# Kernel tuning notes

Measured on AMD Instinct MI355X. Metric: run time of the kernel, lower is better.

## Reference

```python
import jax, jax.numpy as jnp
import numpy as np

BATCH = 16384
NUM_FEATURES = 1024  # sum(field_dims)
CROSS_DIMS = NUM_FEATURES * (NUM_FEATURES - 1) // 2  # 523776


def setup_inputs() -> dict:
    key = jax.random.key(0)
    kx, kw = jax.random.split(key)
    x = jax.random.uniform(kx, (BATCH, NUM_FEATURES), dtype=jnp.float32)
    # xavier-uniform init of a (cross_dims, 1) parameter: bound = sqrt(6/(fan_in+fan_out))
    bound = float(np.sqrt(6.0 / (CROSS_DIMS + 1)))
    w = jax.random.uniform(kw, (CROSS_DIMS,), dtype=jnp.float32, minval=-bound, maxval=bound)
    return {"x": x, "w": w}


def reference(x, w):
    # POLY2: out_b = sigmoid( sum_{i<j} w_{ij} * x_{b,i} * x_{b,j} )
    # sklearn PolynomialFeatures(interaction_only) emits pairs in combinations
    # (row-major i<j) order, identical to triu_indices(k=1) ordering.
    F = x.shape[1]
    iu, ju = jnp.triu_indices(F, k=1)
    W = jnp.zeros((F, F), dtype=x.dtype).at[iu, ju].set(w)  # [F,F] strictly upper-tri
    # quadratic form without materializing the [B, F*(F-1)/2] pairwise matrix
    out = jnp.einsum('bi,ij,bj->b', x, W, x)  # [B]
    return jax.nn.sigmoid(out.astype(jnp.float32))
```

## Files before the change

kernel.cpp:

```cpp
#include <hip/hip_runtime.h>
#include <hip/hip_bf16.h>

#define F 1024
#define B_ROWS 16384

typedef short v8s __attribute__((ext_vector_type(8)));
typedef float v4f __attribute__((ext_vector_type(4)));
typedef unsigned short v8u __attribute__((ext_vector_type(8)));
typedef unsigned short ushort_t;

__device__ __forceinline__ unsigned short f2bf(float f) {
    unsigned int u = __builtin_bit_cast(unsigned int, f);
    u = (u + 0x7FFFu + ((u >> 16) & 1u)) >> 16;
    return (unsigned short)u;
}

__device__ __forceinline__ void gload_lds16(const ushort_t* g, ushort_t* l) {
    __builtin_amdgcn_global_load_lds(
        (const __attribute__((address_space(1))) unsigned int*)g,
        (__attribute__((address_space(3))) unsigned int*)l,
        16, 0, 0);
}


__global__ __launch_bounds__(256) void prep_kernel(
        const float* __restrict__ w, const float* __restrict__ x,
        ushort_t* __restrict__ Bp, ushort_t* __restrict__ Xp,
        float* __restrict__ acc) {
    const int bid  = blockIdx.x;
    const int tid  = threadIdx.x;
    const int lane = tid & 63;
    const int wave = tid >> 6;
    const int l16  = lane & 15;
    const int quad = lane >> 4;

    if (bid < 64) {
        acc[bid * 256 + tid] = 0.0f;
    } else if (bid < 576) {
        const int c  = (bid - 64) * 4 + wave;
        const int n  = (c >> 5) * 16 + l16;
        const int k0 = (c & 31) * 32 + quad * 8;
        v8u o;
#pragma unroll
        for (int e = 0; e < 8; ++e) {
            const int k = k0 + e;
            float v = 0.0f;
            if (k < n) {
                const int idx = k * (F - 1) - (k * (k - 1)) / 2 + (n - k - 1);
                v = w[idx];
            }
            o[e] = f2bf(v);
        }
        *(v8u*)(Bp + (size_t)c * 512 + lane * 8) = o;
    } else {
        const int c  = (bid - 576) * 4 + wave;
        const int r  = (c >> 5) * 16 + l16;
        const int k0 = (c & 31) * 32 + quad * 8;
        const float* src = x + (size_t)r * F + k0;
        float4 v0 = *(const float4*)(src);
        float4 v1 = *(const float4*)(src + 4);
        v8u o;
        o[0] = f2bf(v0.x); o[1] = f2bf(v0.y); o[2] = f2bf(v0.z); o[3] = f2bf(v0.w);
        o[4] = f2bf(v1.x); o[5] = f2bf(v1.y); o[6] = f2bf(v1.z); o[7] = f2bf(v1.w);
        *(v8u*)(Xp + (size_t)c * 512 + lane * 8) = o;
    }
}

__global__ __launch_bounds__(256, 3) void gemm_kernel(
        const ushort_t* __restrict__ Xp,
        const ushort_t* __restrict__ Bp,
        const float*   __restrict__ Xf,
        float*         __restrict__ rowacc) {
    __shared__ ushort_t Bs[2 * 16 * 512];

    const int f   = blockIdx.x;
    const int xcd = f & 7;
    const int g   = f >> 3;
    const int y   = g & 15;
    const int nt  = 7 - (g >> 4);
    const int blockM = (xcd * 16 + y) * 128;
    const int blockN = nt * 128;
    const int nch    = 2 * (nt + 1);

    const int tid   = threadIdx.x;
    const int lane  = tid & 63;
    const int wave  = tid >> 6;
    const int waveM = wave >> 1;
    const int waveN = wave & 1;
    const int quad  = lane >> 4;
    const int l16   = lane & 15;

    const int mg = (blockM >> 4) + waveM * 4;
    const v8s* A8 = (const v8s*)Xp + (size_t)mg * 32 * 64 + lane;

    const int q0   = wave * 4;
    const int ngB  = nt * 8;

#define STAGE_B(c, buf)                                                        \
    {                                                                          \
        _Pragma("unroll")                                                      \
        for (int q = 0; q < 4; ++q) {                                          \
            const int qq  = q0 + q;                                            \
            const int kgl = qq >> 3, ngl = qq & 7;                             \
            gload_lds16(Bp + (size_t)((ngB + ngl) * 32 + (c) * 2 + kgl) * 512 + lane * 8, \
                        Bs + (buf) * 8192 + (kgl * 8 + ngl) * 512);            \
        }                                                                      \
    }

    v4f acc[4][4];
#pragma unroll
    for (int i = 0; i < 4; i++)
#pragma unroll
        for (int j = 0; j < 4; j++) acc[i][j] = (v4f)(0.0f);

    v8s a0[4], a1[4], bfr[4];

    STAGE_B(0, 0)
#pragma unroll
    for (int mi = 0; mi < 4; ++mi) a0[mi] = A8[(mi * 32 + 0) * 64];
    __syncthreads();

    for (int c = 0; c < nch; ++c) {
        const int  buf  = c & 1;
        const bool more = (c + 1 < nch);
        if (more) STAGE_B(c + 1, buf ^ 1)

#pragma unroll
        for (int ni = 0; ni < 4; ++ni)
            bfr[ni] = *(const v8s*)(Bs + buf * 8192 + (0 * 8 + waveN * 4 + ni) * 512 + lane * 8);
#pragma unroll
        for (int mi = 0; mi < 4; ++mi) a1[mi] = A8[(mi * 32 + 2 * c + 1) * 64];
#pragma unroll
        for (int mi = 0; mi < 4; ++mi)
#pragma unroll
            for (int ni = 0; ni < 4; ++ni)
                acc[mi][ni] = __builtin_amdgcn_mfma_f32_16x16x32_bf16(
                    a0[mi], bfr[ni], acc[mi][ni], 0, 0, 0);

#pragma unroll
        for (int ni = 0; ni < 4; ++ni)
            bfr[ni] = *(const v8s*)(Bs + buf * 8192 + (1 * 8 + waveN * 4 + ni) * 512 + lane * 8);
        if (more) {
#pragma unroll
            for (int mi = 0; mi < 4; ++mi) a0[mi] = A8[(mi * 32 + 2 * c + 2) * 64];
        }
#pragma unroll
        for (int mi = 0; mi < 4; ++mi)
#pragma unroll
            for (int ni = 0; ni < 4; ++ni)
                acc[mi][ni] = __builtin_amdgcn_mfma_f32_16x16x32_bf16(
                    a1[mi], bfr[ni], acc[mi][ni], 0, 0, 0);

        if (more) __syncthreads();
    }
#undef STAGE_B

#pragma unroll
    for (int mi = 0; mi < 4; mi++) {
#pragma unroll
        for (int r = 0; r < 4; r++) {
            const int b = blockM + waveM * 64 + mi * 16 + quad * 4 + r;
            const float* xr = Xf + (size_t)b * F + blockN + waveN * 64 + l16;
            float pv = acc[mi][0][r] * xr[0]
                     + acc[mi][1][r] * xr[16]
                     + acc[mi][2][r] * xr[32]
                     + acc[mi][3][r] * xr[48];
            pv += __shfl_xor(pv, 1);
            pv += __shfl_xor(pv, 2);
            pv += __shfl_xor(pv, 4);
            pv += __shfl_xor(pv, 8);
            if (l16 == 0) atomicAdd(&rowacc[b], pv);
        }
    }
}

__global__ void sigmoid_kernel(const float* __restrict__ acc, float* __restrict__ out) {
    int b = blockIdx.x * blockDim.x + threadIdx.x;
    out[b] = 1.0f / (1.0f + __expf(-acc[b]));
}

__global__ void fallback_kernel(const float* __restrict__ x, const float* __restrict__ w,
                                float* __restrict__ out) {
    __shared__ float xs[F];
    __shared__ float partial[4];
    const int b = blockIdx.x;
    for (int i = threadIdx.x; i < F; i += 256) xs[i] = x[(size_t)b * F + i];
    __syncthreads();
    float s = 0.0f;
    for (int i = threadIdx.x; i < F - 1; i += 256) {
        const float xi = xs[i];
        const int kbase = i * (F - 1) - (i * (i - 1)) / 2 - i - 1;
        for (int j = i + 1; j < F; j++) s += w[kbase + j] * xi * xs[j];
    }
    for (int off = 32; off; off >>= 1) s += __shfl_down(s, off);
    if ((threadIdx.x & 63) == 0) partial[threadIdx.x >> 6] = s;
    __syncthreads();
    if (threadIdx.x == 0) {
        float t = partial[0] + partial[1] + partial[2] + partial[3];
        out[b] = 1.0f / (1.0f + __expf(-t));
    }
}

extern "C" void kernel_launch(void* const* d_in, const int* in_sizes, int n_in,
                              void* d_out, int out_size, void* d_ws, size_t ws_size,
                              hipStream_t stream) {
    const float* x = (const float*)d_in[0];
    const float* w = (const float*)d_in[1];
    float* out = (float*)d_out;

    const size_t acc_bytes = 65536;
    const size_t B_bytes   = (size_t)F * F * 2;
    const size_t Xp_bytes  = (size_t)B_ROWS * F * 2;
    const size_t needed = acc_bytes + B_bytes + Xp_bytes;

    if (ws_size < needed) {
        fallback_kernel<<<B_ROWS, 256, 0, stream>>>(x, w, out);
        return;
    }

    float*    acc = (float*)d_ws;
    ushort_t* Bp  = (ushort_t*)((char*)d_ws + acc_bytes);
    ushort_t* Xp  = (ushort_t*)((char*)d_ws + acc_bytes + B_bytes);

    prep_kernel<<<64 + 512 + 8192, 256, 0, stream>>>(w, x, Bp, Xp, acc);
    gemm_kernel<<<1024, 256, 0, stream>>>(Xp, Bp, x, acc);
    sigmoid_kernel<<<B_ROWS / 256, 256, 0, stream>>>(acc, out);
}
```

Before: 133.2 us.

## Fuse sigmoid into GEMM via last-block counter, relax barrier waits, raise occupancy

Removes the separate sigmoid kernel launch: each M row-block keeps a counter, and the last of its 8 N-tile blocks applies the sigmoid and writes the output. In the main loop, the full __syncthreads is replaced by a partial vmcnt wait plus s_barrier, with sched_barriers added to pin the instruction order. Launch bounds rise from 3 to 4 blocks per CU. The changes aim to save a launch and overlap more memory traffic, but they add atomics and fences and risk register spills under the tighter bound.

```diff
diff --git a/kernel.cpp b/kernel.cpp
--- a/kernel.cpp
+++ b/kernel.cpp
@@ -26,7 +26,7 @@
 __global__ __launch_bounds__(256) void prep_kernel(
         const float* __restrict__ w, const float* __restrict__ x,
         ushort_t* __restrict__ Bp, ushort_t* __restrict__ Xp,
-        float* __restrict__ acc) {
+        float* __restrict__ acc, int* __restrict__ cnt) {
     const int bid  = blockIdx.x;
     const int tid  = threadIdx.x;
     const int lane = tid & 63;
@@ -36,8 +36,10 @@
 
     if (bid < 64) {
         acc[bid * 256 + tid] = 0.0f;
-    } else if (bid < 576) {
-        const int c  = (bid - 64) * 4 + wave;
+    } else if (bid == 64) {
+        if (tid < 128) cnt[tid] = 0;
+    } else if (bid < 577) {
+        const int c  = (bid - 65) * 4 + wave;
         const int n  = (c >> 5) * 16 + l16;
         const int k0 = (c & 31) * 32 + quad * 8;
         v8u o;
@@ -53,7 +55,7 @@
         }
         *(v8u*)(Bp + (size_t)c * 512 + lane * 8) = o;
     } else {
-        const int c  = (bid - 576) * 4 + wave;
+        const int c  = (bid - 577) * 4 + wave;
         const int r  = (c >> 5) * 16 + l16;
         const int k0 = (c & 31) * 32 + quad * 8;
         const float* src = x + (size_t)r * F + k0;
@@ -66,12 +68,15 @@
     }
 }
 
-__global__ __launch_bounds__(256, 3) void gemm_kernel(
+__global__ __launch_bounds__(256, 4) void gemm_kernel(
         const ushort_t* __restrict__ Xp,
         const ushort_t* __restrict__ Bp,
         const float*   __restrict__ Xf,
-        float*         __restrict__ rowacc) {
+        float*         __restrict__ rowacc,
+        int*           __restrict__ cnt,
+        float*         __restrict__ outp) {
     __shared__ ushort_t Bs[2 * 16 * 512];
+    __shared__ int lastFlag;
 
     const int f   = blockIdx.x;
     const int xcd = f & 7;
@@ -123,7 +128,10 @@
     for (int c = 0; c < nch; ++c) {
         const int  buf  = c & 1;
         const bool more = (c + 1 < nch);
-        if (more) STAGE_B(c + 1, buf ^ 1)
+        if (more) {
+            STAGE_B(c + 1, buf ^ 1)
+            __builtin_amdgcn_sched_barrier(0);
+        }
 
 #pragma unroll
         for (int ni = 0; ni < 4; ++ni)
@@ -136,6 +144,7 @@
             for (int ni = 0; ni < 4; ++ni)
                 acc[mi][ni] = __builtin_amdgcn_mfma_f32_16x16x32_bf16(
                     a0[mi], bfr[ni], acc[mi][ni], 0, 0, 0);
+        __builtin_amdgcn_sched_barrier(0);
 
 #pragma unroll
         for (int ni = 0; ni < 4; ++ni)
@@ -151,7 +160,12 @@
                 acc[mi][ni] = __builtin_amdgcn_mfma_f32_16x16x32_bf16(
                     a1[mi], bfr[ni], acc[mi][ni], 0, 0, 0);
 
-        if (more) __syncthreads();
+        if (more) {
+            asm volatile("s_waitcnt vmcnt(4)" ::: "memory");
+            __builtin_amdgcn_sched_barrier(0);
+            __builtin_amdgcn_s_barrier();
+            __builtin_amdgcn_sched_barrier(0);
+        }
     }
 #undef STAGE_B
 
@@ -172,11 +186,21 @@
             if (l16 == 0) atomicAdd(&rowacc[b], pv);
         }
     }
-}
-
-__global__ void sigmoid_kernel(const float* __restrict__ acc, float* __restrict__ out) {
-    int b = blockIdx.x * blockDim.x + threadIdx.x;
-    out[b] = 1.0f / (1.0f + __expf(-acc[b]));
+
+    __threadfence();
+    __syncthreads();
+    if (tid == 0) {
+        int old = __hip_atomic_fetch_add(&cnt[blockM >> 7], 1,
+                                         __ATOMIC_ACQ_REL, __HIP_MEMORY_SCOPE_AGENT);
+        lastFlag = (old == 7);
+    }
+    __syncthreads();
+    if (lastFlag && tid < 128) {
+        const int b = blockM + tid;
+        float v = __hip_atomic_load(&rowacc[b], __ATOMIC_RELAXED,
+                                    __HIP_MEMORY_SCOPE_AGENT);
+        outp[b] = 1.0f / (1.0f + __expf(-v));
+    }
 }
 
 __global__ void fallback_kernel(const float* __restrict__ x, const float* __restrict__ w,
@@ -209,9 +233,10 @@
     float* out = (float*)d_out;
 
     const size_t acc_bytes = 65536;
+    const size_t cnt_bytes = 4096;
     const size_t B_bytes   = (size_t)F * F * 2;
     const size_t Xp_bytes  = (size_t)B_ROWS * F * 2;
-    const size_t needed = acc_bytes + B_bytes + Xp_bytes;
+    const size_t needed = acc_bytes + cnt_bytes + B_bytes + Xp_bytes;
 
     if (ws_size < needed) {
         fallback_kernel<<<B_ROWS, 256, 0, stream>>>(x, w, out);
@@ -219,10 +244,10 @@
     }
 
     float*    acc = (float*)d_ws;
-    ushort_t* Bp  = (ushort_t*)((char*)d_ws + acc_bytes);
-    ushort_t* Xp  = (ushort_t*)((char*)d_ws + acc_bytes + B_bytes);
-
-    prep_kernel<<<64 + 512 + 8192, 256, 0, stream>>>(w, x, Bp, Xp, acc);
-    gemm_kernel<<<1024, 256, 0, stream>>>(Xp, Bp, x, acc);
-    sigmoid_kernel<<<B_ROWS / 256, 256, 0, stream>>>(acc, out);
-}
+    int*      cnt = (int*)((char*)d_ws + acc_bytes);
+    ushort_t* Bp  = (ushort_t*)((char*)d_ws + acc_bytes + cnt_bytes);
+    ushort_t* Xp  = (ushort_t*)((char*)d_ws + acc_bytes + cnt_bytes + B_bytes);
+
+    prep_kernel<<<64 + 1 + 512 + 8192, 256, 0, stream>>>(w, x, Bp, Xp, acc, cnt);
+    gemm_kernel<<<1024, 256, 0, stream>>>(Xp, Bp, x, acc, cnt, out);
+}
```

New measurement: 260.2 us. +95.4%, slower.
